# Kernel optimization log

Measured on AMD Instinct MI355X. Metric: run time of the kernel, lower is better.

## Reference

```python
import jax, jax.numpy as jnp
import numpy as np

T, G, K, N = 131072, 64, 1024, 512  # batch_sum, batch_count, k, n
M_MAX = 4096  # static upper bound on any group size (setup guarantees <= 3072)
PAD = 128     # tile alignment for padded offsets


def setup_inputs() -> dict:
    key = jax.random.key(0)
    k1, k2 = jax.random.split(key)
    a = jax.random.normal(k1, (T, K), dtype=jnp.float32)
    b = jax.random.normal(k2, (G, K, N), dtype=jnp.float32) / np.float32(np.sqrt(K))
    rng = np.random.default_rng(0)
    d = rng.integers(-1024, 1024, G // 2)
    deltas = np.concatenate([d, -d])
    rng.shuffle(deltas)
    sizes = (T // G) + deltas  # each in [1024, 3072], sums exactly to T
    offsets = np.concatenate([[0], np.cumsum(sizes)[:-1]])
    padded = ((sizes + PAD - 1) // PAD) * PAD
    padded_offsets = np.concatenate([[0], np.cumsum(padded)[:-1]])
    return {
        "a": a,
        "b": b,
        "batch_sizes": jnp.asarray(sizes, dtype=jnp.int32),
        "batch_offsets": jnp.asarray(offsets, dtype=jnp.int32),
        "batch_padded_offsets": jnp.asarray(padded_offsets, dtype=jnp.int32),
    }


def reference(a, b, batch_sizes, batch_offsets, batch_padded_offsets):
    # Grouped GEMM: for each group g, out[off_g : off_g+size_g] = a[rows] @ b[g].
    # jit-friendly: scan over groups with a fixed M_MAX window, mask invalid rows.
    T_, _ = a.shape
    n_out = b.shape[-1]
    iota = jnp.arange(M_MAX)

    def body(out, xs):
        off, size, bg = xs
        rows = jnp.clip(off + iota, 0, T_ - 1)          # [M_MAX]
        mask = iota < size                               # [M_MAX]
        a_g = jnp.where(mask[:, None], a[rows], 0.0)     # [M_MAX, K]
        y = a_g @ bg                                     # [M_MAX, N]
        out = out.at[rows].add(y)                        # masked rows add zeros
        return out, None

    out0 = jnp.zeros((T_, n_out), dtype=a.dtype)
    out, _ = jax.lax.scan(body, out0, (batch_offsets, batch_sizes, b))
    return out
```

## Files before the change

kernel.cpp:

```cpp
#include <hip/hip_runtime.h>
#include <hip/hip_bf16.h>
#include <stdint.h>

#define T_ROWS 131072
#define GCNT   64
#define KDIM   1024
#define NDIM   512
#define BM     128
#define BN     128
#define BK     32
#define KTILES (KDIM / BK)
#define MT_MAX 1088
#define NBLK   (MT_MAX * 4)

typedef __attribute__((ext_vector_type(4))) float f32x4;
typedef __attribute__((ext_vector_type(8))) short s16x8;
typedef __attribute__((ext_vector_type(4))) short s16x4;
typedef __attribute__((address_space(3))) unsigned int lds_u32;
typedef const __attribute__((address_space(1))) unsigned int gbl_u32;

static __device__ __forceinline__ short f2bf(float f) {
  __hip_bfloat16 h = __float2bfloat16(f);
  return __builtin_bit_cast(short, h);
}

__global__ __launch_bounds__(256) void bt_kernel(const float* __restrict__ b,
                                                 char* __restrict__ bt) {
  __shared__ short lt[32 * 130];
  int bid = blockIdx.x;
  int kt = bid & 31, nt = (bid >> 5) & 3, g = bid >> 7;
  int t = threadIdx.x;
  const float* src = b + ((size_t)(g * KDIM + kt * BK)) * NDIM + nt * 128;
#pragma unroll
  for (int i = 0; i < 16; i++) {
    int idx = i * 256 + t;
    int kk = idx >> 7, nn = idx & 127;
    lt[kk * 130 + nn] = f2bf(src[(size_t)kk * NDIM + nn]);
  }
  __syncthreads();
  char* dst = bt + ((size_t)bid << 13);
#pragma unroll
  for (int j = 0; j < 2; j++) {
    int chunk = j * 256 + t;
    int n = chunk >> 2;
    int s8 = (chunk & 3) ^ ((n >> 1) & 3);
    s16x8 v;
#pragma unroll
    for (int i = 0; i < 8; i++) v[i] = lt[(s8 * 8 + i) * 130 + n];
    *(s16x8*)(dst + (size_t)chunk * 16) = v;
  }
}

__global__ __launch_bounds__(256, 4) void gemm5(
    const float* __restrict__ a, const char* __restrict__ bt,
    const int* __restrict__ sizes, const int* __restrict__ offs,
    float* __restrict__ out) {
  __shared__ __align__(16) short lds_a[BM * BK];
  __shared__ __align__(16) char lds_b[2][BN * BK * 2];

  int bid0 = blockIdx.x;
  int bid = (bid0 & 7) * (NBLK / 8) + (bid0 >> 3);
  int bn = bid & 3;
  int tm = bid >> 2;

  int g = -1, m_loc = 0, base = 0;
#pragma unroll
  for (int i = 0; i < GCNT; i++) {
    int tg = ((sizes[i] + 127) & ~127) >> 7;
    if (tm >= base && tm < base + tg) { g = i; m_loc = (tm - base) << 7; }
    base += tg;
  }
  if (g < 0) return;
  int size = sizes[g], off = offs[g], valid = size - m_loc;

  int t = threadIdx.x, lane = t & 63, wid = t >> 6;
  int wm = wid >> 1, wn = wid & 1, lr = lane & 15, q = lane >> 4;

  int ar = t >> 1, ah = t & 1;
  {
    int row = off + m_loc + ar;
    if (row >= T_ROWS) row = T_ROWS - 1;
    ar = row;
  }
  const float* abase = a + (size_t)ar * KDIM + ah * 16;
  int arl = t >> 1;
  int aslot0 = (ah * 2) ^ ((arl >> 1) & 3);
  int aslot1 = (ah * 2 + 1) ^ ((arl >> 1) & 3);
  char* awb = (char*)lds_a + arl * 64;

  const char* btimg = bt + ((size_t)((g << 7) + (bn << 5)) << 13);

  f32x4 acc[4][4];
#pragma unroll
  for (int i = 0; i < 4; i++)
#pragma unroll
    for (int j = 0; j < 4; j++) acc[i][j] = (f32x4){0.f, 0.f, 0.f, 0.f};
  f32x4 va[4];

  auto loadA = [&](int kt) {
#pragma unroll
    for (int i = 0; i < 4; i++)
      va[i] = *(const f32x4*)(abase + kt * BK + i * 4);
  };
  auto writeA = [&]() {
    s16x8 w0, w1;
#pragma unroll
    for (int e = 0; e < 4; e++) {
      w0[e] = f2bf(va[0][e]);
      w0[4 + e] = f2bf(va[1][e]);
      w1[e] = f2bf(va[2][e]);
      w1[4 + e] = f2bf(va[3][e]);
    }
    *(s16x8*)(awb + aslot0 * 16) = w0;
    *(s16x8*)(awb + aslot1 * 16) = w1;
  };
  auto stageB = [&](int kt, int c) {
#pragma unroll
    for (int i = 0; i < 2; i++) {
      int wc = wid * 2 + i;
      int cc = wc * 64 + lane;
      const char* gsrc = btimg + ((size_t)kt << 13) + (size_t)cc * 16;
      __builtin_amdgcn_global_load_lds(
          (gbl_u32*)gsrc, (lds_u32*)((char*)lds_b[c] + wc * 1024), 16, 0, 0);
    }
  };
  auto compute = [&](int c) {
    s16x8 af[4], bf[4];
#pragma unroll
    for (int fm = 0; fm < 4; fm++) {
      int row = wm * 64 + fm * 16 + lr;
      int slot = q ^ ((row >> 1) & 3);
      af[fm] = *(const s16x8*)((const char*)lds_a + row * 64 + slot * 16);
    }
#pragma unroll
    for (int fn = 0; fn < 4; fn++) {
      int n = wn * 64 + fn * 16 + lr;
      int slot = q ^ ((n >> 1) & 3);
      bf[fn] = *(const s16x8*)((const char*)lds_b[c] + n * 64 + slot * 16);
    }
    __builtin_amdgcn_s_setprio(1);
#pragma unroll
    for (int fm = 0; fm < 4; fm++)
#pragma unroll
      for (int fn = 0; fn < 4; fn++)
        acc[fm][fn] = __builtin_amdgcn_mfma_f32_16x16x32_bf16(
            af[fm], bf[fn], acc[fm][fn], 0, 0, 0);
    __builtin_amdgcn_s_setprio(0);
  };

  stageB(0, 0);
  __builtin_amdgcn_sched_barrier(0);
  loadA(0);

  for (int kt = 0; kt < KTILES - 1; kt++) {
    int cur = kt & 1, nxt = cur ^ 1;
    stageB(kt + 1, nxt);
    __builtin_amdgcn_sched_barrier(0);
    writeA();
    loadA(kt + 1);
    asm volatile("s_waitcnt lgkmcnt(0)" ::: "memory");
    __builtin_amdgcn_s_barrier();
    compute(cur);
    __builtin_amdgcn_s_barrier();
  }
  writeA();
  asm volatile("s_waitcnt lgkmcnt(0)" ::: "memory");
  __builtin_amdgcn_s_barrier();
  compute(1);

  size_t orow0 = (size_t)(off + m_loc);
#pragma unroll
  for (int fm = 0; fm < 4; fm++) {
#pragma unroll
    for (int j = 0; j < 4; j++) {
      int rm = wm * 64 + fm * 16 + q * 4 + j;
      if (rm < valid) {
        float* orow = out + (orow0 + rm) * NDIM + bn * BN + wn * 64 + lr;
#pragma unroll
        for (int fn = 0; fn < 4; fn++) orow[fn * 16] = acc[fm][fn][j];
      }
    }
  }
}

__global__ __launch_bounds__(256, 2) void gemm_fb(
    const float* __restrict__ a, const float* __restrict__ b,
    const int* __restrict__ sizes, const int* __restrict__ offs,
    float* __restrict__ out) {
  __shared__ __align__(16) short lds_a2[2][128 * 64];
  __shared__ __align__(16) char lds_b2[2][128 * 64 * 2];

  int bid0 = blockIdx.x;
  int bid = (bid0 & 7) * (NBLK / 8) + (bid0 >> 3);
  int bn = bid & 3;
  int tm = bid >> 2;

  int g = -1, m_loc = 0, base = 0;
#pragma unroll
  for (int i = 0; i < GCNT; i++) {
    int tg = ((sizes[i] + 127) & ~127) >> 7;
    if (tm >= base && tm < base + tg) { g = i; m_loc = (tm - base) << 7; }
    base += tg;
  }
  if (g < 0) return;
  int size = sizes[g], off = offs[g], valid = size - m_loc;

  int t = threadIdx.x, lane = t & 63, wid = t >> 6;
  int wm = wid >> 1, wn = wid & 1, lr = lane & 15, q = lane >> 4;

  int r0 = t >> 4, c16 = t & 15;
  int aoff[8];
#pragma unroll
  for (int i = 0; i < 8; i++) {
    int row = off + m_loc + i * 16 + r0;
    if (row >= T_ROWS) row = T_ROWS - 1;
    aoff[i] = row * KDIM + c16 * 4;
  }
  int a_wbyte = r0 * 128 + (((c16 >> 1) ^ (r0 & 7)) << 4) + (c16 & 1) * 8;
  int fb_n = t >> 1, fb_kh = (t & 1) * 32;

  f32x4 acc[4][4];
#pragma unroll
  for (int i = 0; i < 4; i++)
#pragma unroll
    for (int j = 0; j < 4; j++) acc[i][j] = (f32x4){0.f, 0.f, 0.f, 0.f};
  f32x4 va[8];

  auto loadA = [&](int kt) {
#pragma unroll
    for (int i = 0; i < 8; i++)
      va[i] = *(const f32x4*)(a + aoff[i] + kt * 64);
  };
  auto writeA = [&](int c) {
    char* db = (char*)lds_a2[c] + a_wbyte;
#pragma unroll
    for (int i = 0; i < 8; i++) {
      s16x4 v;
#pragma unroll
      for (int e = 0; e < 4; e++) v[e] = f2bf(va[i][e]);
      *(s16x4*)(db + i * 2048) = v;
    }
  };
  auto stageB = [&](int kt, int c) {
    const float* p = b + (size_t)g * KDIM * NDIM +
                     (size_t)(kt * 64 + fb_kh) * NDIM + bn * 128 + fb_n;
    float vals[32];
#pragma unroll
    for (int i = 0; i < 32; i++) vals[i] = p[(size_t)i * NDIM];
    char* lb = (char*)lds_b2[c] + fb_n * 128;
#pragma unroll
    for (int i8 = 0; i8 < 4; i8++) {
      int slot = (fb_kh >> 3) + i8;
      s16x8 v;
#pragma unroll
      for (int e = 0; e < 8; e++) v[e] = f2bf(vals[i8 * 8 + e]);
      *(s16x8*)(lb + ((slot ^ (fb_n & 7)) << 4)) = v;
    }
  };
  auto compute = [&](int c) {
#pragma unroll
    for (int ks = 0; ks < 2; ks++) {
      s16x8 af[4], bf[4];
#pragma unroll
      for (int fm = 0; fm < 4; fm++) {
        int row = wm * 64 + fm * 16 + lr;
        int slot = (ks * 4 + q) ^ (row & 7);
        af[fm] =
            *(const s16x8*)((const char*)lds_a2[c] + row * 128 + slot * 16);
      }
#pragma unroll
      for (int fn = 0; fn < 4; fn++) {
        int n = wn * 64 + fn * 16 + lr;
        int slot = (ks * 4 + q) ^ (n & 7);
        bf[fn] = *(const s16x8*)((const char*)lds_b2[c] + n * 128 + slot * 16);
      }
#pragma unroll
      for (int fm = 0; fm < 4; fm++)
#pragma unroll
        for (int fn = 0; fn < 4; fn++)
          acc[fm][fn] = __builtin_amdgcn_mfma_f32_16x16x32_bf16(
              af[fm], bf[fn], acc[fm][fn], 0, 0, 0);
    }
  };

  loadA(0);
  stageB(0, 0);
  writeA(0);
  __syncthreads();
  for (int kt = 0; kt < 16; kt++) {
    int cur = kt & 1, nxt = cur ^ 1;
    bool more = (kt + 1 < 16);
    if (more) loadA(kt + 1);
    compute(cur);
    if (more) {
      stageB(kt + 1, nxt);
      writeA(nxt);
      __syncthreads();
    }
  }
  size_t orow0 = (size_t)(off + m_loc);
#pragma unroll
  for (int fm = 0; fm < 4; fm++) {
#pragma unroll
    for (int j = 0; j < 4; j++) {
      int rm = wm * 64 + fm * 16 + q * 4 + j;
      if (rm < valid) {
        float* orow = out + (orow0 + rm) * NDIM + bn * 128 + wn * 64 + lr;
#pragma unroll
        for (int fn = 0; fn < 4; fn++) orow[fn * 16] = acc[fm][fn][j];
      }
    }
  }
}

extern "C" void kernel_launch(void* const* d_in, const int* in_sizes, int n_in,
                              void* d_out, int out_size, void* d_ws,
                              size_t ws_size, hipStream_t stream) {
  const float* a = (const float*)d_in[0];
  const float* b = (const float*)d_in[1];
  const int* sizes = (const int*)d_in[2];
  const int* offs = (const int*)d_in[3];
  float* out = (float*)d_out;

  const size_t bt_bytes = (size_t)GCNT * KDIM * NDIM * 2;
  if (ws_size >= bt_bytes) {
    bt_kernel<<<GCNT * 128, 256, 0, stream>>>(b, (char*)d_ws);
    gemm5<<<NBLK, 256, 0, stream>>>(a, (const char*)d_ws, sizes, offs, out);
  } else {
    gemm_fb<<<NBLK, 256, 0, stream>>>(a, b, sizes, offs, out);
  }
}
```

Before: 332.8 us.

## Stage fp32 A tiles via direct global-to-LDS DMA with double buffering

After: 342.5 us. 1.03x slower.

```diff
diff --git a/kernel.cpp b/kernel.cpp
--- a/kernel.cpp
+++ b/kernel.cpp
@@ -15,7 +15,6 @@
 
 typedef __attribute__((ext_vector_type(4))) float f32x4;
 typedef __attribute__((ext_vector_type(8))) short s16x8;
-typedef __attribute__((ext_vector_type(4))) short s16x4;
 typedef __attribute__((address_space(3))) unsigned int lds_u32;
 typedef const __attribute__((address_space(1))) unsigned int gbl_u32;
 
@@ -51,11 +50,11 @@
   }
 }
 
-__global__ __launch_bounds__(256, 4) void gemm5(
+__global__ __launch_bounds__(256, 3) void gemm6(
     const float* __restrict__ a, const char* __restrict__ bt,
     const int* __restrict__ sizes, const int* __restrict__ offs,
     float* __restrict__ out) {
-  __shared__ __align__(16) short lds_a[BM * BK];
+  __shared__ __align__(16) float lds_a[2][BM * BK];
   __shared__ __align__(16) char lds_b[2][BN * BK * 2];
 
   int bid0 = blockIdx.x;
@@ -76,17 +75,16 @@
   int t = threadIdx.x, lane = t & 63, wid = t >> 6;
   int wm = wid >> 1, wn = wid & 1, lr = lane & 15, q = lane >> 4;
 
-  int ar = t >> 1, ah = t & 1;
-  {
-    int row = off + m_loc + ar;
+  int adma[4];
+#pragma unroll
+  for (int j = 0; j < 4; j++) {
+    int rloc = (wid * 4 + j) * 8 + (lane >> 3);
+    int row = off + m_loc + rloc;
     if (row >= T_ROWS) row = T_ROWS - 1;
-    ar = row;
-  }
-  const float* abase = a + (size_t)ar * KDIM + ah * 16;
-  int arl = t >> 1;
-  int aslot0 = (ah * 2) ^ ((arl >> 1) & 3);
-  int aslot1 = (ah * 2 + 1) ^ ((arl >> 1) & 3);
-  char* awb = (char*)lds_a + arl * 64;
+    int cs = (lane & 7) ^ (rloc & 7);
+    adma[j] = row * (KDIM * 4) + cs * 16;
+  }
+  const char* a8 = (const char*)a;
 
   const char* btimg = bt + ((size_t)((g << 7) + (bn << 5)) << 13);
 
@@ -95,24 +93,15 @@
   for (int i = 0; i < 4; i++)
 #pragma unroll
     for (int j = 0; j < 4; j++) acc[i][j] = (f32x4){0.f, 0.f, 0.f, 0.f};
-  f32x4 va[4];
-
-  auto loadA = [&](int kt) {
-#pragma unroll
-    for (int i = 0; i < 4; i++)
-      va[i] = *(const f32x4*)(abase + kt * BK + i * 4);
-  };
-  auto writeA = [&]() {
-    s16x8 w0, w1;
-#pragma unroll
-    for (int e = 0; e < 4; e++) {
-      w0[e] = f2bf(va[0][e]);
-      w0[4 + e] = f2bf(va[1][e]);
-      w1[e] = f2bf(va[2][e]);
-      w1[4 + e] = f2bf(va[3][e]);
-    }
-    *(s16x8*)(awb + aslot0 * 16) = w0;
-    *(s16x8*)(awb + aslot1 * 16) = w1;
+
+  auto stageA = [&](int kt, int c) {
+#pragma unroll
+    for (int j = 0; j < 4; j++) {
+      const char* gsrc = a8 + adma[j] + kt * (BK * 4);
+      char* ldst = (char*)lds_a[c] + (wid * 4 + j) * 1024;
+      __builtin_amdgcn_global_load_lds((gbl_u32*)gsrc, (lds_u32*)ldst, 16, 0,
+                                       0);
+    }
   };
   auto stageB = [&](int kt, int c) {
 #pragma unroll
@@ -129,8 +118,16 @@
 #pragma unroll
     for (int fm = 0; fm < 4; fm++) {
       int row = wm * 64 + fm * 16 + lr;
-      int slot = q ^ ((row >> 1) & 3);
-      af[fm] = *(const s16x8*)((const char*)lds_a + row * 64 + slot * 16);
+      const char* rp = (const char*)lds_a[c] + row * 128;
+      f32x4 lo = *(const f32x4*)(rp + (((q * 2) ^ (row & 7)) << 4));
+      f32x4 hi = *(const f32x4*)(rp + (((q * 2 + 1) ^ (row & 7)) << 4));
+      s16x8 v;
+#pragma unroll
+      for (int e = 0; e < 4; e++) {
+        v[e] = f2bf(lo[e]);
+        v[4 + e] = f2bf(hi[e]);
+      }
+      af[fm] = v;
     }
 #pragma unroll
     for (int fn = 0; fn < 4; fn++) {
@@ -148,25 +145,24 @@
     __builtin_amdgcn_s_setprio(0);
   };
 
+  stageA(0, 0);
   stageB(0, 0);
-  __builtin_amdgcn_sched_barrier(0);
-  loadA(0);
-
-  for (int kt = 0; kt < KTILES - 1; kt++) {
+  asm volatile("s_waitcnt vmcnt(0)" ::: "memory");
+  __builtin_amdgcn_s_barrier();
+
+  for (int kt = 0; kt < KTILES; kt++) {
     int cur = kt & 1, nxt = cur ^ 1;
-    stageB(kt + 1, nxt);
-    __builtin_amdgcn_sched_barrier(0);
-    writeA();
-    loadA(kt + 1);
-    asm volatile("s_waitcnt lgkmcnt(0)" ::: "memory");
-    __builtin_amdgcn_s_barrier();
+    bool more = (kt + 1 < KTILES);
+    if (more) {
+      stageA(kt + 1, nxt);
+      stageB(kt + 1, nxt);
+    }
     compute(cur);
-    __builtin_amdgcn_s_barrier();
-  }
-  writeA();
-  asm volatile("s_waitcnt lgkmcnt(0)" ::: "memory");
-  __builtin_amdgcn_s_barrier();
-  compute(1);
+    if (more) {
+      asm volatile("s_waitcnt vmcnt(0)" ::: "memory");
+      __builtin_amdgcn_s_barrier();
+    }
+  }
 
   size_t orow0 = (size_t)(off + m_loc);
 #pragma unroll
@@ -182,6 +178,8 @@
     }
   }
 }
+
+typedef __attribute__((ext_vector_type(4))) short s16x4;
 
 __global__ __launch_bounds__(256, 2) void gemm_fb(
     const float* __restrict__ a, const float* __restrict__ b,
@@ -325,7 +323,7 @@
   const size_t bt_bytes = (size_t)GCNT * KDIM * NDIM * 2;
   if (ws_size >= bt_bytes) {
     bt_kernel<<<GCNT * 128, 256, 0, stream>>>(b, (char*)d_ws);
-    gemm5<<<NBLK, 256, 0, stream>>>(a, (const char*)d_ws, sizes, offs, out);
+    gemm6<<<NBLK, 256, 0, stream>>>(a, (const char*)d_ws, sizes, offs, out);
   } else {
     gemm_fb<<<NBLK, 256, 0, stream>>>(a, b, sizes, offs, out);
   }
```
